# Optimization experiments

Measured on AMD Instinct MI355X. Metric: run time of the kernel, lower is better.

The kernel has to match this reference:

```python
import jax, jax.numpy as jnp
import numpy as np
from jax import lax

E = 4      # n_experts
K = 2      # top_k
D = 1024   # d_model
B, S = 4, 4096


def setup_inputs() -> dict:
    key = jax.random.key(0)
    ks = jax.random.split(key, 9)
    sc = 1.0 / np.sqrt(D)
    x = jax.random.normal(ks[0], (B, S, D), dtype=jnp.float32)
    Wg = jax.random.normal(ks[1], (E, D, D), dtype=jnp.float32) * sc
    bg = jax.random.normal(ks[2], (E, D), dtype=jnp.float32) * sc
    Wv = jax.random.normal(ks[3], (E, D, D), dtype=jnp.float32) * sc
    bv = jax.random.normal(ks[4], (E, D), dtype=jnp.float32) * sc
    Wd = jax.random.normal(ks[5], (E, D, D), dtype=jnp.float32) * sc
    # decay_bias_init = 1.0 (torch init.constant_)
    bd = jnp.ones((E, D), dtype=jnp.float32)
    Wgate = jax.random.normal(ks[7], (E, D), dtype=jnp.float32) * sc
    return {"x": x, "Wg": Wg, "bg": bg, "Wv": Wv, "bv": bv,
            "Wd": Wd, "bd": bd, "Wgate": Wgate}


def reference(x, Wg, bg, Wv, bv, Wd, bd, Wgate):
    # Per-expert projections (torch Linear: y = x @ W.T + b; W is (out,in))
    g = jnp.einsum('bsd,eod->ebso', x, Wg) + bg[:, None, None, :]  # (E,B,S,D)
    v = jnp.einsum('bsd,eod->ebso', x, Wv) + bv[:, None, None, :]
    d = jnp.einsum('bsd,eod->ebso', x, Wd) + bd[:, None, None, :]
    x_scan = jax.nn.sigmoid(g) * jnp.tanh(v)
    a = 0.001 + 0.998 * jax.nn.sigmoid(d)

    # Causal linear RNN: h_t = a_t * h_{t-1} + x_t, vectorized over (E,B,D)
    xs = jnp.moveaxis(x_scan, 2, 0)  # (S,E,B,D)
    as_ = jnp.moveaxis(a, 2, 0)      # (S,E,B,D)

    def step(h, inp):
        a_t, x_t = inp
        h = a_t * h + x_t
        return h, h

    h0 = jnp.zeros((E, B, x.shape[-1]), dtype=x.dtype)
    _, outs = lax.scan(step, h0, (as_, xs))        # (S,E,B,D)
    expert_outs = jnp.transpose(outs, (2, 0, 3, 1))  # (B,S,D,E)

    # Router: top-k experts per token, softmax over selected logits
    gate_logits = jnp.einsum('bsd,ed->bse', x, Wgate)  # (B,S,E)
    top_vals, top_idx = lax.top_k(gate_logits, K)      # (B,S,K)
    weights = jax.nn.softmax(top_vals, axis=-1)        # (B,S,K)

    idx = jnp.broadcast_to(top_idx[:, :, None, :],
                           (x.shape[0], x.shape[1], x.shape[2], K))
    selected = jnp.take_along_axis(expert_outs, idx, axis=-1)  # (B,S,D,K)
    return (selected * weights[:, :, None, :]).sum(axis=-1)
```

## Files before the change

### kernel.cpp

```cpp
#include <hip/hip_runtime.h>

#define E_EXP 4
#define D_MODEL 1024
#define B_BATCH 4
#define S_SEQ 4096
#define NTOK (B_BATCH*S_SEQ)
#define CHUNK 32
#define NCHUNK (S_SEQ/CHUNK)

typedef float f4 __attribute__((ext_vector_type(4)));
typedef float f32x4 __attribute__((ext_vector_type(4)));
typedef short bf16x8 __attribute__((ext_vector_type(8)));

__device__ __forceinline__ unsigned short f2b(float f){
  union{float f;unsigned u;}v; v.f=f;
  unsigned r = v.u + 0x7fffu + ((v.u>>16)&1u);
  return (unsigned short)(r>>16);
}
__device__ __forceinline__ float b2f_us(unsigned short v){ union{unsigned u;float f;}x; x.u=((unsigned)v)<<16; return x.f; }
__device__ __forceinline__ float b2f_lo(unsigned v){ union{unsigned u;float f;}x; x.u=v<<16; return x.f; }
__device__ __forceinline__ float b2f_hi(unsigned v){ union{unsigned u;float f;}x; x.u=v&0xffff0000u; return x.f; }

__device__ __forceinline__ void gload_lds16(const void* g, void* l){
  __builtin_amdgcn_global_load_lds(
      (const __attribute__((address_space(1))) void*)g,
      (__attribute__((address_space(3))) void*)l, 16, 0, 0);
}

__global__ __launch_bounds__(256) void cvt_bf16(const float* __restrict__ src,
                                                unsigned short* __restrict__ dst)
{
  size_t i = ((size_t)blockIdx.x*256 + threadIdx.x)*4;
  f4 v = *(const f4*)(src + i);
  ushort4 o; o.x=f2b(v[0]); o.y=f2b(v[1]); o.z=f2b(v[2]); o.w=f2b(v[3]);
  *(ushort4*)(dst + i) = o;
}

__global__ __launch_bounds__(256) void router_kernel(
    const float* __restrict__ x, const float* __restrict__ Wgate,
    float* __restrict__ wtok)
{
  int gtid = blockIdx.x*256 + threadIdx.x;
  int tok  = gtid >> 6;
  int lane = threadIdx.x & 63;
  const float* xr = x + (size_t)tok * D_MODEL;
  float acc0=0.f,acc1=0.f,acc2=0.f,acc3=0.f;
  for (int k=lane;k<D_MODEL;k+=64){
    float xv = xr[k];
    acc0 += xv*Wgate[0*D_MODEL+k];
    acc1 += xv*Wgate[1*D_MODEL+k];
    acc2 += xv*Wgate[2*D_MODEL+k];
    acc3 += xv*Wgate[3*D_MODEL+k];
  }
  #pragma unroll
  for (int off=32;off>0;off>>=1){
    acc0 += __shfl_down(acc0,off);
    acc1 += __shfl_down(acc1,off);
    acc2 += __shfl_down(acc2,off);
    acc3 += __shfl_down(acc3,off);
  }
  if (lane==0){
    float l[4]={acc0,acc1,acc2,acc3};
    int i1=0;
    #pragma unroll
    for(int e=1;e<4;e++) if (l[e]>l[i1]) i1=e;
    int i2=-1;
    #pragma unroll
    for(int e=0;e<4;e++){ if(e==i1) continue; if(i2<0||l[e]>l[i2]) i2=e; }
    float ex = __expf(l[i2]-l[i1]);
    float w1 = 1.f/(1.f+ex);
    float w2 = ex/(1.f+ex);
    float w[4]={0.f,0.f,0.f,0.f};
    w[i1]=w1; w[i2]=w2;
    float* wp = wtok + (size_t)tok*E_EXP;
    wp[0]=w[0]; wp[1]=w[1]; wp[2]=w[2]; wp[3]=w[3];
  }
}

#define BM 128
#define BN 128
#define BK 32

template<int EPI>
__global__ __launch_bounds__(256) void gemm_bf16(
    const unsigned short* __restrict__ A,
    const unsigned short* __restrict__ W,
    const float* __restrict__ bias,
    const unsigned short* __restrict__ gsrc,
    unsigned short* __restrict__ dst,
    int e0)
{
  __shared__ unsigned short sA[BM*BK];
  __shared__ unsigned short sB[BN*BK];
  int le = blockIdx.z;
  int mbase = blockIdx.x*BM, nbase = blockIdx.y*BN;
  int tid  = threadIdx.x;
  int wave = tid>>6, lane = tid&63;
  int wm = wave>>1, wn = wave&1;

  const unsigned short* We = W + (size_t)le*D_MODEL*D_MODEL;

  int srow = wave*32 + (lane>>2);
  int scol = (lane&3)*8;
  const unsigned short* gA0 = A  + (size_t)(mbase+srow)*D_MODEL + scol;
  const unsigned short* gA1 = gA0 + (size_t)16*D_MODEL;
  const unsigned short* gB0 = We + (size_t)(nbase+srow)*D_MODEL + scol;
  const unsigned short* gB1 = gB0 + (size_t)16*D_MODEL;
  unsigned short* lA0 = &sA[(wave*32)*BK];
  unsigned short* lA1 = &sA[(wave*32+16)*BK];
  unsigned short* lB0 = &sB[(wave*32)*BK];
  unsigned short* lB1 = &sB[(wave*32+16)*BK];

  f32x4 acc[4][4];
  #pragma unroll
  for (int i=0;i<4;i++)
    #pragma unroll
    for (int j=0;j<4;j++) acc[i][j] = 0;

  int arow = wm*64 + (lane&15);
  int brow = wn*64 + (lane&15);
  int kfr  = (lane>>4)*8;

  for (int k0=0; k0<D_MODEL; k0+=BK){
    gload_lds16(gA0 + k0, lA0);
    gload_lds16(gA1 + k0, lA1);
    gload_lds16(gB0 + k0, lB0);
    gload_lds16(gB1 + k0, lB1);
    __syncthreads();
    bf16x8 af[4], bfv[4];
    #pragma unroll
    for (int mi=0;mi<4;mi++) af[mi]  = *(const bf16x8*)&sA[(arow + mi*16)*BK + kfr];
    #pragma unroll
    for (int ni=0;ni<4;ni++) bfv[ni] = *(const bf16x8*)&sB[(brow + ni*16)*BK + kfr];
    #pragma unroll
    for (int mi=0;mi<4;mi++)
      #pragma unroll
      for (int ni=0;ni<4;ni++)
        acc[mi][ni] = __builtin_amdgcn_mfma_f32_16x16x32_bf16(af[mi], bfv[ni], acc[mi][ni], 0, 0, 0);
    __syncthreads();
  }

  const float* be = bias + (size_t)(e0+le)*D_MODEL;
  int me = mbase + wm*64;
  int ne = nbase + wn*64;
  #pragma unroll
  for (int mi=0;mi<4;mi++){
    #pragma unroll
    for (int r=0;r<4;r++){
      int m = me + mi*16 + (lane>>4)*4 + r;
      size_t rowoff = ((size_t)le*NTOK + m)*D_MODEL;
      #pragma unroll
      for (int ni=0;ni<4;ni++){
        int n = ne + ni*16 + (lane&15);
        float val = acc[mi][ni][r] + be[n];
        float res;
        if (EPI==0){
          res = val;
        } else if (EPI==1){
          float g  = b2f_us(gsrc[rowoff+n]);
          float sg = 1.f/(1.f+__expf(-g));
          float th = 1.f - 2.f/(__expf(2.f*val)+1.f);
          res = sg*th;
        } else {
          res = 0.001f + 0.998f/(1.f+__expf(-val));
        }
        dst[rowoff+n] = f2b(res);
      }
    }
  }
}

__global__ __launch_bounds__(512) void scan_pass1(
    const unsigned short* __restrict__ xs, const unsigned short* __restrict__ aa,
    float* __restrict__ P, float* __restrict__ U)
{
  int blk = blockIdx.x;
  int c  = blk % NCHUNK;
  int b  = (blk / NCHUNK) % B_BATCH;
  int le = blk / (NCHUNK*B_BATCH);
  int d0 = threadIdx.x*2;
  size_t base = (((size_t)(le*B_BATCH + b))*S_SEQ + (size_t)c*CHUNK)*D_MODEL + d0;
  float h0=0.f,h1=0.f,p0=1.f,p1=1.f;
  #pragma unroll 4
  for (int t=0;t<CHUNK;t++){
    unsigned av = *(const unsigned*)(aa + base);
    unsigned xv = *(const unsigned*)(xs + base);
    float a0=b2f_lo(av), a1=b2f_hi(av);
    float x0=b2f_lo(xv), x1=b2f_hi(xv);
    h0 = a0*h0 + x0; h1 = a1*h1 + x1;
    p0 *= a0; p1 *= a1;
    base += D_MODEL;
  }
  size_t sidx = (((size_t)(le*B_BATCH + b))*NCHUNK + c)*D_MODEL + d0;
  P[sidx]=p0; P[sidx+1]=p1;
  U[sidx]=h0; U[sidx+1]=h1;
}

__global__ __launch_bounds__(256) void scan_pass2(
    const float* __restrict__ P, const float* __restrict__ U, float* __restrict__ Hinit)
{
  int ch = blockIdx.x*256 + threadIdx.x;
  int d  = ch & (D_MODEL-1);
  int eb = ch >> 10;
  size_t base = (size_t)eb*NCHUNK*D_MODEL + d;
  float H=0.f;
  for (int c=0;c<NCHUNK;c++){
    size_t idx = base + (size_t)c*D_MODEL;
    Hinit[idx] = H;
    H = P[idx]*H + U[idx];
  }
}

template<int G>
__global__ __launch_bounds__(512) void scan_pass3(
    const unsigned short* __restrict__ xs, const unsigned short* __restrict__ aa,
    const float* __restrict__ Hinit, const float* __restrict__ wtok,
    float* __restrict__ out, int e0)
{
  int blk = blockIdx.x;
  int c = blk % NCHUNK;
  int b = blk / NCHUNK;
  int d0 = threadIdx.x*2;
  float h[G][2];
  #pragma unroll
  for (int le=0; le<G; le++){
    size_t hi = (((size_t)(le*B_BATCH+b))*NCHUNK + c)*D_MODEL + d0;
    h[le][0]=Hinit[hi]; h[le][1]=Hinit[hi+1];
  }
  int s0 = c*CHUNK;
  for (int t=0;t<CHUNK;t++){
    size_t n = (size_t)b*S_SEQ + s0 + t;
    float o0=0.f, o1=0.f;
    #pragma unroll
    for (int le=0;le<G;le++){
      float w = wtok[n*E_EXP + e0 + le];
      size_t idx = (((size_t)(le*B_BATCH+b))*S_SEQ + (size_t)(s0 + t))*D_MODEL + d0;
      unsigned av = *(const unsigned*)(aa+idx);
      unsigned xv = *(const unsigned*)(xs+idx);
      h[le][0] = b2f_lo(av)*h[le][0] + b2f_lo(xv);
      h[le][1] = b2f_hi(av)*h[le][1] + b2f_hi(xv);
      o0 += w*h[le][0];
      o1 += w*h[le][1];
    }
    float* op = out + n*D_MODEL + d0;
    if (G == E_EXP){ op[0]=o0; op[1]=o1; }
    else           { op[0]+=o0; op[1]+=o1; }
  }
}

extern "C" void kernel_launch(void* const* d_in, const int* in_sizes, int n_in,
                              void* d_out, int out_size, void* d_ws, size_t ws_size,
                              hipStream_t stream)
{
  const float* x     = (const float*)d_in[0];
  const float* Wg    = (const float*)d_in[1];
  const float* bg    = (const float*)d_in[2];
  const float* Wv    = (const float*)d_in[3];
  const float* bv    = (const float*)d_in[4];
  const float* Wd    = (const float*)d_in[5];
  const float* bd    = (const float*)d_in[6];
  const float* Wgate = (const float*)d_in[7];
  float* out = (float*)d_out;

  const size_t DD       = (size_t)D_MODEL*D_MODEL;
  const size_t wtok_b   = (size_t)NTOK*E_EXP*4;
  const size_t xbf_b    = (size_t)NTOK*D_MODEL*2;
  const size_t w_per_e  = DD*2;
  const size_t xs_per_e = (size_t)NTOK*D_MODEL*2;
  const size_t st_per_e = (size_t)B_BATCH*NCHUNK*D_MODEL*4;

  int G = 1;
  for (int g = 4; g >= 1; g >>= 1){
    size_t need = wtok_b + xbf_b + (size_t)g*(3*w_per_e + 2*xs_per_e + 3*st_per_e);
    if (need <= ws_size){ G = g; break; }
  }

  char* wsb = (char*)d_ws;
  size_t off = 0;
  float*          wtok = (float*)(wsb+off);          off += wtok_b;
  unsigned short* xbf  = (unsigned short*)(wsb+off); off += xbf_b;
  unsigned short* Wgbf = (unsigned short*)(wsb+off); off += (size_t)G*w_per_e;
  unsigned short* Wvbf = (unsigned short*)(wsb+off); off += (size_t)G*w_per_e;
  unsigned short* Wdbf = (unsigned short*)(wsb+off); off += (size_t)G*w_per_e;
  unsigned short* xs   = (unsigned short*)(wsb+off); off += (size_t)G*xs_per_e;
  unsigned short* aa   = (unsigned short*)(wsb+off); off += (size_t)G*xs_per_e;
  float*          P    = (float*)(wsb+off);          off += (size_t)G*st_per_e;
  float*          U    = (float*)(wsb+off);          off += (size_t)G*st_per_e;
  float*          Hi   = (float*)(wsb+off);

  hipMemsetAsync(d_out, 0, (size_t)out_size*sizeof(float), stream);

  cvt_bf16<<<(unsigned)((size_t)NTOK*D_MODEL/1024), 256, 0, stream>>>(x, xbf);
  router_kernel<<<NTOK/4, 256, 0, stream>>>(x, Wgate, wtok);

  for (int e0=0; e0<E_EXP; e0+=G){
    cvt_bf16<<<(unsigned)((size_t)G*DD/1024), 256, 0, stream>>>(Wg + (size_t)e0*DD, Wgbf);
    cvt_bf16<<<(unsigned)((size_t)G*DD/1024), 256, 0, stream>>>(Wv + (size_t)e0*DD, Wvbf);
    cvt_bf16<<<(unsigned)((size_t)G*DD/1024), 256, 0, stream>>>(Wd + (size_t)e0*DD, Wdbf);

    dim3 gg(NTOK/BM, D_MODEL/BN, G);
    gemm_bf16<0><<<gg, 256, 0, stream>>>(xbf, Wgbf, bg, nullptr, aa, e0);
    gemm_bf16<1><<<gg, 256, 0, stream>>>(xbf, Wvbf, bv, aa, xs, e0);
    gemm_bf16<2><<<gg, 256, 0, stream>>>(xbf, Wdbf, bd, nullptr, aa, e0);

    scan_pass1<<<G*B_BATCH*NCHUNK, 512, 0, stream>>>(xs, aa, P, U);
    scan_pass2<<<G*B_BATCH*D_MODEL/256, 256, 0, stream>>>(P, U, Hi);
    if (G==4)      scan_pass3<4><<<B_BATCH*NCHUNK, 512, 0, stream>>>(xs, aa, Hi, wtok, out, e0);
    else if (G==2) scan_pass3<2><<<B_BATCH*NCHUNK, 512, 0, stream>>>(xs, aa, Hi, wtok, out, e0);
    else           scan_pass3<1><<<B_BATCH*NCHUNK, 512, 0, stream>>>(xs, aa, Hi, wtok, out, e0);
  }
}
```

Baseline: 956.3 us.

## Fuse gate/value/decay GEMMs into one kernel sharing A tiles

Replaces three separate per-projection GEMMs with a single kernel that loads each x tile once and computes the g, v and d accumulators together, with BN halved to 64 to hold register pressure. The epilogue computes both the scan input and the decay directly, so the g intermediate is no longer written and re-read, and aa is not written twice. The weights are converted into an interleaved per-expert concatenated buffer. It also drops the output memset by making the first expert group overwrite rather than accumulate. The cost is three accumulator sets per thread and more LDS per block, which may lower occupancy.

```diff
diff --git a/kernel.cpp b/kernel.cpp
--- a/kernel.cpp
+++ b/kernel.cpp
@@ -17,7 +17,6 @@
   unsigned r = v.u + 0x7fffu + ((v.u>>16)&1u);
   return (unsigned short)(r>>16);
 }
-__device__ __forceinline__ float b2f_us(unsigned short v){ union{unsigned u;float f;}x; x.u=((unsigned)v)<<16; return x.f; }
 __device__ __forceinline__ float b2f_lo(unsigned v){ union{unsigned u;float f;}x; x.u=v<<16; return x.f; }
 __device__ __forceinline__ float b2f_hi(unsigned v){ union{unsigned u;float f;}x; x.u=v&0xffff0000u; return x.f; }
 
@@ -34,6 +33,18 @@
   f4 v = *(const f4*)(src + i);
   ushort4 o; o.x=f2b(v[0]); o.y=f2b(v[1]); o.z=f2b(v[2]); o.w=f2b(v[3]);
   *(ushort4*)(dst + i) = o;
+}
+
+__global__ __launch_bounds__(256) void cvt_w(const float* __restrict__ W,
+                                             unsigned short* __restrict__ Wcat,
+                                             int e0, int mat)
+{
+  size_t i4 = ((size_t)blockIdx.x*256 + threadIdx.x)*4;
+  size_t le  = i4 >> 20;
+  size_t rem = i4 & ((1u<<20)-1);
+  f4 v = *(const f4*)(W + (size_t)(e0+le)*D_MODEL*D_MODEL + rem);
+  ushort4 o; o.x=f2b(v[0]); o.y=f2b(v[1]); o.z=f2b(v[2]); o.w=f2b(v[3]);
+  *(ushort4*)(Wcat + (le*3 + mat)*((size_t)D_MODEL*D_MODEL) + rem) = o;
 }
 
 __global__ __launch_bounds__(256) void router_kernel(
@@ -78,47 +89,49 @@
 }
 
 #define BM 128
-#define BN 128
+#define BN 64
 #define BK 32
 
-template<int EPI>
-__global__ __launch_bounds__(256) void gemm_bf16(
+__global__ __launch_bounds__(256) void gemm_fused(
     const unsigned short* __restrict__ A,
-    const unsigned short* __restrict__ W,
-    const float* __restrict__ bias,
-    const unsigned short* __restrict__ gsrc,
-    unsigned short* __restrict__ dst,
+    const unsigned short* __restrict__ Wcat,
+    const float* __restrict__ bg, const float* __restrict__ bv,
+    const float* __restrict__ bd,
+    unsigned short* __restrict__ xs, unsigned short* __restrict__ aa,
     int e0)
 {
   __shared__ unsigned short sA[BM*BK];
-  __shared__ unsigned short sB[BN*BK];
+  __shared__ unsigned short sB[3*BN*BK];
   int le = blockIdx.z;
   int mbase = blockIdx.x*BM, nbase = blockIdx.y*BN;
   int tid  = threadIdx.x;
   int wave = tid>>6, lane = tid&63;
   int wm = wave>>1, wn = wave&1;
 
-  const unsigned short* We = W + (size_t)le*D_MODEL*D_MODEL;
-
-  int srow = wave*32 + (lane>>2);
+  const size_t DD = (size_t)D_MODEL*D_MODEL;
+  const unsigned short* We = Wcat + (size_t)le*3*DD;
+
+  int srow = lane>>2;
   int scol = (lane&3)*8;
-  const unsigned short* gA0 = A  + (size_t)(mbase+srow)*D_MODEL + scol;
-  const unsigned short* gA1 = gA0 + (size_t)16*D_MODEL;
-  const unsigned short* gB0 = We + (size_t)(nbase+srow)*D_MODEL + scol;
-  const unsigned short* gB1 = gB0 + (size_t)16*D_MODEL;
-  unsigned short* lA0 = &sA[(wave*32)*BK];
-  unsigned short* lA1 = &sA[(wave*32+16)*BK];
-  unsigned short* lB0 = &sB[(wave*32)*BK];
-  unsigned short* lB1 = &sB[(wave*32+16)*BK];
-
-  f32x4 acc[4][4];
+  const unsigned short* gA0 = A + (size_t)(mbase + wave*16 + srow)*D_MODEL + scol;
+  const unsigned short* gA1 = gA0 + (size_t)64*D_MODEL;
+  const unsigned short* gB0 = We + 0*DD + (size_t)(nbase + wave*16 + srow)*D_MODEL + scol;
+  const unsigned short* gB1 = We + 1*DD + (size_t)(nbase + wave*16 + srow)*D_MODEL + scol;
+  const unsigned short* gB2 = We + 2*DD + (size_t)(nbase + wave*16 + srow)*D_MODEL + scol;
+  unsigned short* lA0 = &sA[(wave*16)*BK];
+  unsigned short* lA1 = &sA[(wave*16+64)*BK];
+  unsigned short* lB0 = &sB[0*BN*BK + (wave*16)*BK];
+  unsigned short* lB1 = &sB[1*BN*BK + (wave*16)*BK];
+  unsigned short* lB2 = &sB[2*BN*BK + (wave*16)*BK];
+
+  f32x4 accG[4][2], accV[4][2], accD[4][2];
   #pragma unroll
   for (int i=0;i<4;i++)
     #pragma unroll
-    for (int j=0;j<4;j++) acc[i][j] = 0;
+    for (int j=0;j<2;j++){ accG[i][j]=0; accV[i][j]=0; accD[i][j]=0; }
 
   int arow = wm*64 + (lane&15);
-  int brow = wn*64 + (lane&15);
+  int brow = wn*32 + (lane&15);
   int kfr  = (lane>>4)*8;
 
   for (int k0=0; k0<D_MODEL; k0+=BK){
@@ -126,23 +139,32 @@
     gload_lds16(gA1 + k0, lA1);
     gload_lds16(gB0 + k0, lB0);
     gload_lds16(gB1 + k0, lB1);
+    gload_lds16(gB2 + k0, lB2);
     __syncthreads();
-    bf16x8 af[4], bfv[4];
-    #pragma unroll
-    for (int mi=0;mi<4;mi++) af[mi]  = *(const bf16x8*)&sA[(arow + mi*16)*BK + kfr];
-    #pragma unroll
-    for (int ni=0;ni<4;ni++) bfv[ni] = *(const bf16x8*)&sB[(brow + ni*16)*BK + kfr];
-    #pragma unroll
-    for (int mi=0;mi<4;mi++)
+    bf16x8 af[4];
+    #pragma unroll
+    for (int mi=0;mi<4;mi++) af[mi] = *(const bf16x8*)&sA[(arow + mi*16)*BK + kfr];
+    #pragma unroll
+    for (int ni=0;ni<2;ni++){
+      bf16x8 b0 = *(const bf16x8*)&sB[0*BN*BK + (brow + ni*16)*BK + kfr];
+      bf16x8 b1 = *(const bf16x8*)&sB[1*BN*BK + (brow + ni*16)*BK + kfr];
+      bf16x8 b2 = *(const bf16x8*)&sB[2*BN*BK + (brow + ni*16)*BK + kfr];
       #pragma unroll
-      for (int ni=0;ni<4;ni++)
-        acc[mi][ni] = __builtin_amdgcn_mfma_f32_16x16x32_bf16(af[mi], bfv[ni], acc[mi][ni], 0, 0, 0);
+      for (int mi=0;mi<4;mi++){
+        accG[mi][ni] = __builtin_amdgcn_mfma_f32_16x16x32_bf16(af[mi], b0, accG[mi][ni], 0, 0, 0);
+        accV[mi][ni] = __builtin_amdgcn_mfma_f32_16x16x32_bf16(af[mi], b1, accV[mi][ni], 0, 0, 0);
+        accD[mi][ni] = __builtin_amdgcn_mfma_f32_16x16x32_bf16(af[mi], b2, accD[mi][ni], 0, 0, 0);
+      }
+    }
     __syncthreads();
   }
 
-  const float* be = bias + (size_t)(e0+le)*D_MODEL;
+  int e = e0 + le;
+  const float* bge = bg + (size_t)e*D_MODEL;
+  const float* bve = bv + (size_t)e*D_MODEL;
+  const float* bde = bd + (size_t)e*D_MODEL;
   int me = mbase + wm*64;
-  int ne = nbase + wn*64;
+  int ne = nbase + wn*32;
   #pragma unroll
   for (int mi=0;mi<4;mi++){
     #pragma unroll
@@ -150,21 +172,16 @@
       int m = me + mi*16 + (lane>>4)*4 + r;
       size_t rowoff = ((size_t)le*NTOK + m)*D_MODEL;
       #pragma unroll
-      for (int ni=0;ni<4;ni++){
+      for (int ni=0;ni<2;ni++){
         int n = ne + ni*16 + (lane&15);
-        float val = acc[mi][ni][r] + be[n];
-        float res;
-        if (EPI==0){
-          res = val;
-        } else if (EPI==1){
-          float g  = b2f_us(gsrc[rowoff+n]);
-          float sg = 1.f/(1.f+__expf(-g));
-          float th = 1.f - 2.f/(__expf(2.f*val)+1.f);
-          res = sg*th;
-        } else {
-          res = 0.001f + 0.998f/(1.f+__expf(-val));
-        }
-        dst[rowoff+n] = f2b(res);
+        float g = accG[mi][ni][r] + bge[n];
+        float v = accV[mi][ni][r] + bve[n];
+        float d = accD[mi][ni][r] + bde[n];
+        float sg = 1.f/(1.f+__expf(-g));
+        float th = 1.f - 2.f/(__expf(2.f*v)+1.f);
+        float av = 0.001f + 0.998f/(1.f+__expf(-d));
+        xs[rowoff+n] = f2b(sg*th);
+        aa[rowoff+n] = f2b(av);
       }
     }
   }
@@ -211,7 +228,7 @@
   }
 }
 
-template<int G>
+template<int G, int FIRST>
 __global__ __launch_bounds__(512) void scan_pass3(
     const unsigned short* __restrict__ xs, const unsigned short* __restrict__ aa,
     const float* __restrict__ Hinit, const float* __restrict__ wtok,
@@ -243,8 +260,8 @@
       o1 += w*h[le][1];
     }
     float* op = out + n*D_MODEL + d0;
-    if (G == E_EXP){ op[0]=o0; op[1]=o1; }
-    else           { op[0]+=o0; op[1]+=o1; }
+    if (FIRST){ op[0]=o0;  op[1]=o1;  }
+    else      { op[0]+=o0; op[1]+=o1; }
   }
 }
 
@@ -265,13 +282,13 @@
   const size_t DD       = (size_t)D_MODEL*D_MODEL;
   const size_t wtok_b   = (size_t)NTOK*E_EXP*4;
   const size_t xbf_b    = (size_t)NTOK*D_MODEL*2;
-  const size_t w_per_e  = DD*2;
+  const size_t w_per_e  = 3*DD*2;
   const size_t xs_per_e = (size_t)NTOK*D_MODEL*2;
   const size_t st_per_e = (size_t)B_BATCH*NCHUNK*D_MODEL*4;
 
   int G = 1;
   for (int g = 4; g >= 1; g >>= 1){
-    size_t need = wtok_b + xbf_b + (size_t)g*(3*w_per_e + 2*xs_per_e + 3*st_per_e);
+    size_t need = wtok_b + xbf_b + (size_t)g*(w_per_e + 2*xs_per_e + 3*st_per_e);
     if (need <= ws_size){ G = g; break; }
   }
 
@@ -279,34 +296,35 @@
   size_t off = 0;
   float*          wtok = (float*)(wsb+off);          off += wtok_b;
   unsigned short* xbf  = (unsigned short*)(wsb+off); off += xbf_b;
-  unsigned short* Wgbf = (unsigned short*)(wsb+off); off += (size_t)G*w_per_e;
-  unsigned short* Wvbf = (unsigned short*)(wsb+off); off += (size_t)G*w_per_e;
-  unsigned short* Wdbf = (unsigned short*)(wsb+off); off += (size_t)G*w_per_e;
+  unsigned short* Wcat = (unsigned short*)(wsb+off); off += (size_t)G*w_per_e;
   unsigned short* xs   = (unsigned short*)(wsb+off); off += (size_t)G*xs_per_e;
   unsigned short* aa   = (unsigned short*)(wsb+off); off += (size_t)G*xs_per_e;
   float*          P    = (float*)(wsb+off);          off += (size_t)G*st_per_e;
   float*          U    = (float*)(wsb+off);          off += (size_t)G*st_per_e;
   float*          Hi   = (float*)(wsb+off);
 
-  hipMemsetAsync(d_out, 0, (size_t)out_size*sizeof(float), stream);
-
   cvt_bf16<<<(unsigned)((size_t)NTOK*D_MODEL/1024), 256, 0, stream>>>(x, xbf);
   router_kernel<<<NTOK/4, 256, 0, stream>>>(x, Wgate, wtok);
 
   for (int e0=0; e0<E_EXP; e0+=G){
-    cvt_bf16<<<(unsigned)((size_t)G*DD/1024), 256, 0, stream>>>(Wg + (size_t)e0*DD, Wgbf);
-    cvt_bf16<<<(unsigned)((size_t)G*DD/1024), 256, 0, stream>>>(Wv + (size_t)e0*DD, Wvbf);
-    cvt_bf16<<<(unsigned)((size_t)G*DD/1024), 256, 0, stream>>>(Wd + (size_t)e0*DD, Wdbf);
+    unsigned cvg = (unsigned)((size_t)G*DD/1024);
+    cvt_w<<<cvg, 256, 0, stream>>>(Wg, Wcat, e0, 0);
+    cvt_w<<<cvg, 256, 0, stream>>>(Wv, Wcat, e0, 1);
+    cvt_w<<<cvg, 256, 0, stream>>>(Wd, Wcat, e0, 2);
 
     dim3 gg(NTOK/BM, D_MODEL/BN, G);
-    gemm_bf16<0><<<gg, 256, 0, stream>>>(xbf, Wgbf, bg, nullptr, aa, e0);
-    gemm_bf16<1><<<gg, 256, 0, stream>>>(xbf, Wvbf, bv, aa, xs, e0);
-    gemm_bf16<2><<<gg, 256, 0, stream>>>(xbf, Wdbf, bd, nullptr, aa, e0);
+    gemm_fused<<<gg, 256, 0, stream>>>(xbf, Wcat, bg, bv, bd, xs, aa, e0);
 
     scan_pass1<<<G*B_BATCH*NCHUNK, 512, 0, stream>>>(xs, aa, P, U);
     scan_pass2<<<G*B_BATCH*D_MODEL/256, 256, 0, stream>>>(P, U, Hi);
-    if (G==4)      scan_pass3<4><<<B_BATCH*NCHUNK, 512, 0, stream>>>(xs, aa, Hi, wtok, out, e0);
-    else if (G==2) scan_pass3<2><<<B_BATCH*NCHUNK, 512, 0, stream>>>(xs, aa, Hi, wtok, out, e0);
-    else           scan_pass3<1><<<B_BATCH*NCHUNK, 512, 0, stream>>>(xs, aa, Hi, wtok, out, e0);
-  }
-}
+    bool first = (e0 == 0);
+    if (G==4)      scan_pass3<4,1><<<B_BATCH*NCHUNK, 512, 0, stream>>>(xs, aa, Hi, wtok, out, e0);
+    else if (G==2){
+      if (first) scan_pass3<2,1><<<B_BATCH*NCHUNK, 512, 0, stream>>>(xs, aa, Hi, wtok, out, e0);
+      else       scan_pass3<2,0><<<B_BATCH*NCHUNK, 512, 0, stream>>>(xs, aa, Hi, wtok, out, e0);
+    } else {
+      if (first) scan_pass3<1,1><<<B_BATCH*NCHUNK, 512, 0, stream>>>(xs, aa, Hi, wtok, out, e0);
+      else       scan_pass3<1,0><<<B_BATCH*NCHUNK, 512, 0, stream>>>(xs, aa, Hi, wtok, out, e0);
+    }
+  }
+}
```

New measurement: 1.359 ms. 42.1% more time.

## Fuse three projection GEMMs into one, move activations into scan pass

Applied to the files above, without the earlier changes.

Concatenates the Wg/Wv/Wd bf16 weights and runs a single GEMM over 3×D output columns that writes raw bf16 pre-activations. Bias, sigmoid/tanh gating and the decay activation now run inside scan_pass1, which writes xs and a back in place. The GEMM also gains an XOR-swizzled LDS layout to avoid bank conflicts. The output memset is dropped by having the first expert group store instead of accumulate. The aim is fewer launches, no gsrc re-read in the epilogue and a simpler GEMM epilogue. The cost is an extra bf16 tensor (g, v, d stored separately) and more transcendental work in the scan pass.

```diff
diff --git a/kernel.cpp b/kernel.cpp
--- a/kernel.cpp
+++ b/kernel.cpp
@@ -17,7 +17,6 @@
   unsigned r = v.u + 0x7fffu + ((v.u>>16)&1u);
   return (unsigned short)(r>>16);
 }
-__device__ __forceinline__ float b2f_us(unsigned short v){ union{unsigned u;float f;}x; x.u=((unsigned)v)<<16; return x.f; }
 __device__ __forceinline__ float b2f_lo(unsigned v){ union{unsigned u;float f;}x; x.u=v<<16; return x.f; }
 __device__ __forceinline__ float b2f_hi(unsigned v){ union{unsigned u;float f;}x; x.u=v&0xffff0000u; return x.f; }
 
@@ -34,6 +33,24 @@
   f4 v = *(const f4*)(src + i);
   ushort4 o; o.x=f2b(v[0]); o.y=f2b(v[1]); o.z=f2b(v[2]); o.w=f2b(v[3]);
   *(ushort4*)(dst + i) = o;
+}
+
+__global__ __launch_bounds__(256) void cvt_w3(const float* __restrict__ Wg,
+                                              const float* __restrict__ Wv,
+                                              const float* __restrict__ Wd,
+                                              unsigned short* __restrict__ Wcat,
+                                              int e0)
+{
+  const size_t DD = (size_t)D_MODEL*D_MODEL;
+  size_t i4 = ((size_t)blockIdx.x*256 + threadIdx.x)*4;
+  size_t le3m = i4 >> 20;
+  size_t rem  = i4 & (DD-1);
+  int mat = (int)(le3m % 3);
+  int le  = (int)(le3m / 3);
+  const float* src = (mat==0 ? Wg : (mat==1 ? Wv : Wd)) + (size_t)(e0+le)*DD + rem;
+  f4 v = *(const f4*)src;
+  ushort4 o; o.x=f2b(v[0]); o.y=f2b(v[1]); o.z=f2b(v[2]); o.w=f2b(v[3]);
+  *(ushort4*)(Wcat + le3m*DD + rem) = o;
 }
 
 __global__ __launch_bounds__(256) void router_kernel(
@@ -81,31 +98,33 @@
 #define BN 128
 #define BK 32
 
-template<int EPI>
-__global__ __launch_bounds__(256) void gemm_bf16(
+__global__ __launch_bounds__(256) void gemm_3n(
     const unsigned short* __restrict__ A,
-    const unsigned short* __restrict__ W,
-    const float* __restrict__ bias,
-    const unsigned short* __restrict__ gsrc,
-    unsigned short* __restrict__ dst,
-    int e0)
+    const unsigned short* __restrict__ Wcat,
+    unsigned short* __restrict__ gvd)
 {
   __shared__ unsigned short sA[BM*BK];
   __shared__ unsigned short sB[BN*BK];
-  int le = blockIdx.z;
-  int mbase = blockIdx.x*BM, nbase = blockIdx.y*BN;
+  const size_t DD = (size_t)D_MODEL*D_MODEL;
+  const size_t ND = (size_t)NTOK*D_MODEL;
+
+  int le    = blockIdx.z;
+  int mbase = blockIdx.x*BM;
+  int ntile = blockIdx.y;
+  int mat   = ntile>>3;
+  int nbase = (ntile&7)*BN;
   int tid  = threadIdx.x;
   int wave = tid>>6, lane = tid&63;
   int wm = wave>>1, wn = wave&1;
 
-  const unsigned short* We = W + (size_t)le*D_MODEL*D_MODEL;
-
-  int srow = wave*32 + (lane>>2);
-  int scol = (lane&3)*8;
-  const unsigned short* gA0 = A  + (size_t)(mbase+srow)*D_MODEL + scol;
-  const unsigned short* gA1 = gA0 + (size_t)16*D_MODEL;
-  const unsigned short* gB0 = We + (size_t)(nbase+srow)*D_MODEL + scol;
-  const unsigned short* gB1 = gB0 + (size_t)16*D_MODEL;
+  const unsigned short* Wmat = Wcat + ((size_t)le*3 + mat)*DD;
+
+  int src_chunk = (lane&3) ^ ((lane>>3)&3);
+  int srow = lane>>2;
+  const unsigned short* gA0 = A    + (size_t)(mbase + wave*32 + srow)*D_MODEL + src_chunk*8;
+  const unsigned short* gA1 = gA0  + (size_t)16*D_MODEL;
+  const unsigned short* gB0 = Wmat + (size_t)(nbase + wave*32 + srow)*D_MODEL + src_chunk*8;
+  const unsigned short* gB1 = gB0  + (size_t)16*D_MODEL;
   unsigned short* lA0 = &sA[(wave*32)*BK];
   unsigned short* lA1 = &sA[(wave*32+16)*BK];
   unsigned short* lB0 = &sB[(wave*32)*BK];
@@ -117,9 +136,10 @@
     #pragma unroll
     for (int j=0;j<4;j++) acc[i][j] = 0;
 
-  int arow = wm*64 + (lane&15);
-  int brow = wn*64 + (lane&15);
-  int kfr  = (lane>>4)*8;
+  int swiz   = (lane>>1)&3;
+  int rd_chk = ((lane>>4) ^ swiz)*8;
+  int a_base = (wm*64 + (lane&15))*BK + rd_chk;
+  int b_base = (wn*64 + (lane&15))*BK + rd_chk;
 
   for (int k0=0; k0<D_MODEL; k0+=BK){
     gload_lds16(gA0 + k0, lA0);
@@ -129,9 +149,9 @@
     __syncthreads();
     bf16x8 af[4], bfv[4];
     #pragma unroll
-    for (int mi=0;mi<4;mi++) af[mi]  = *(const bf16x8*)&sA[(arow + mi*16)*BK + kfr];
-    #pragma unroll
-    for (int ni=0;ni<4;ni++) bfv[ni] = *(const bf16x8*)&sB[(brow + ni*16)*BK + kfr];
+    for (int mi=0;mi<4;mi++) af[mi]  = *(const bf16x8*)&sA[a_base + mi*16*BK];
+    #pragma unroll
+    for (int ni=0;ni<4;ni++) bfv[ni] = *(const bf16x8*)&sB[b_base + ni*16*BK];
     #pragma unroll
     for (int mi=0;mi<4;mi++)
       #pragma unroll
@@ -140,7 +160,7 @@
     __syncthreads();
   }
 
-  const float* be = bias + (size_t)(e0+le)*D_MODEL;
+  unsigned short* outp = gvd + ((size_t)le*3 + mat)*ND;
   int me = mbase + wm*64;
   int ne = nbase + wn*64;
   #pragma unroll
@@ -148,47 +168,53 @@
     #pragma unroll
     for (int r=0;r<4;r++){
       int m = me + mi*16 + (lane>>4)*4 + r;
-      size_t rowoff = ((size_t)le*NTOK + m)*D_MODEL;
+      size_t rowoff = (size_t)m*D_MODEL;
       #pragma unroll
       for (int ni=0;ni<4;ni++){
         int n = ne + ni*16 + (lane&15);
-        float val = acc[mi][ni][r] + be[n];
-        float res;
-        if (EPI==0){
-          res = val;
-        } else if (EPI==1){
-          float g  = b2f_us(gsrc[rowoff+n]);
-          float sg = 1.f/(1.f+__expf(-g));
-          float th = 1.f - 2.f/(__expf(2.f*val)+1.f);
-          res = sg*th;
-        } else {
-          res = 0.001f + 0.998f/(1.f+__expf(-val));
-        }
-        dst[rowoff+n] = f2b(res);
+        outp[rowoff+n] = f2b(acc[mi][ni][r]);
       }
     }
   }
 }
 
 __global__ __launch_bounds__(512) void scan_pass1(
-    const unsigned short* __restrict__ xs, const unsigned short* __restrict__ aa,
-    float* __restrict__ P, float* __restrict__ U)
-{
+    unsigned short* __restrict__ gvd,
+    const float* __restrict__ bg, const float* __restrict__ bv, const float* __restrict__ bd,
+    float* __restrict__ P, float* __restrict__ U, int e0)
+{
+  const size_t ND = (size_t)NTOK*D_MODEL;
   int blk = blockIdx.x;
   int c  = blk % NCHUNK;
   int b  = (blk / NCHUNK) % B_BATCH;
   int le = blk / (NCHUNK*B_BATCH);
   int d0 = threadIdx.x*2;
-  size_t base = (((size_t)(le*B_BATCH + b))*S_SEQ + (size_t)c*CHUNK)*D_MODEL + d0;
+  int e  = e0 + le;
+
+  float bg0 = bg[(size_t)e*D_MODEL+d0], bg1 = bg[(size_t)e*D_MODEL+d0+1];
+  float bv0 = bv[(size_t)e*D_MODEL+d0], bv1 = bv[(size_t)e*D_MODEL+d0+1];
+  float bd0 = bd[(size_t)e*D_MODEL+d0], bd1 = bd[(size_t)e*D_MODEL+d0+1];
+
+  unsigned short* gp = gvd + (size_t)le*3*ND;
+  size_t base = (((size_t)b)*S_SEQ + (size_t)c*CHUNK)*D_MODEL + d0;
   float h0=0.f,h1=0.f,p0=1.f,p1=1.f;
-  #pragma unroll 4
   for (int t=0;t<CHUNK;t++){
-    unsigned av = *(const unsigned*)(aa + base);
-    unsigned xv = *(const unsigned*)(xs + base);
-    float a0=b2f_lo(av), a1=b2f_hi(av);
-    float x0=b2f_lo(xv), x1=b2f_hi(xv);
+    unsigned gw = *(const unsigned*)(gp + base);
+    unsigned vw = *(const unsigned*)(gp + ND + base);
+    unsigned dw = *(const unsigned*)(gp + 2*ND + base);
+    float g0 = b2f_lo(gw)+bg0, g1 = b2f_hi(gw)+bg1;
+    float v0 = b2f_lo(vw)+bv0, v1 = b2f_hi(vw)+bv1;
+    float dd0 = b2f_lo(dw)+bd0, dd1 = b2f_hi(dw)+bd1;
+    float x0 = (1.f/(1.f+__expf(-g0))) * (1.f - 2.f/(__expf(2.f*v0)+1.f));
+    float x1 = (1.f/(1.f+__expf(-g1))) * (1.f - 2.f/(__expf(2.f*v1)+1.f));
+    float a0 = 0.001f + 0.998f/(1.f+__expf(-dd0));
+    float a1 = 0.001f + 0.998f/(1.f+__expf(-dd1));
     h0 = a0*h0 + x0; h1 = a1*h1 + x1;
     p0 *= a0; p1 *= a1;
+    unsigned xsw = (unsigned)f2b(x0) | ((unsigned)f2b(x1)<<16);
+    unsigned aaw = (unsigned)f2b(a0) | ((unsigned)f2b(a1)<<16);
+    *(unsigned*)(gp + base)        = xsw;
+    *(unsigned*)(gp + 2*ND + base) = aaw;
     base += D_MODEL;
   }
   size_t sidx = (((size_t)(le*B_BATCH + b))*NCHUNK + c)*D_MODEL + d0;
@@ -211,12 +237,13 @@
   }
 }
 
-template<int G>
+template<int G, int FIRST>
 __global__ __launch_bounds__(512) void scan_pass3(
-    const unsigned short* __restrict__ xs, const unsigned short* __restrict__ aa,
+    const unsigned short* __restrict__ gvd,
     const float* __restrict__ Hinit, const float* __restrict__ wtok,
     float* __restrict__ out, int e0)
 {
+  const size_t ND = (size_t)NTOK*D_MODEL;
   int blk = blockIdx.x;
   int c = blk % NCHUNK;
   int b = blk / NCHUNK;
@@ -234,17 +261,17 @@
     #pragma unroll
     for (int le=0;le<G;le++){
       float w = wtok[n*E_EXP + e0 + le];
-      size_t idx = (((size_t)(le*B_BATCH+b))*S_SEQ + (size_t)(s0 + t))*D_MODEL + d0;
-      unsigned av = *(const unsigned*)(aa+idx);
-      unsigned xv = *(const unsigned*)(xs+idx);
+      size_t idx = (size_t)le*3*ND + n*D_MODEL + d0;
+      unsigned xv = *(const unsigned*)(gvd + idx);
+      unsigned av = *(const unsigned*)(gvd + 2*ND + idx);
       h[le][0] = b2f_lo(av)*h[le][0] + b2f_lo(xv);
       h[le][1] = b2f_hi(av)*h[le][1] + b2f_hi(xv);
       o0 += w*h[le][0];
       o1 += w*h[le][1];
     }
     float* op = out + n*D_MODEL + d0;
-    if (G == E_EXP){ op[0]=o0; op[1]=o1; }
-    else           { op[0]+=o0; op[1]+=o1; }
+    if (FIRST){ op[0]=o0;  op[1]=o1;  }
+    else      { op[0]+=o0; op[1]+=o1; }
   }
 }
 
@@ -262,16 +289,17 @@
   const float* Wgate = (const float*)d_in[7];
   float* out = (float*)d_out;
 
-  const size_t DD       = (size_t)D_MODEL*D_MODEL;
-  const size_t wtok_b   = (size_t)NTOK*E_EXP*4;
-  const size_t xbf_b    = (size_t)NTOK*D_MODEL*2;
-  const size_t w_per_e  = DD*2;
-  const size_t xs_per_e = (size_t)NTOK*D_MODEL*2;
-  const size_t st_per_e = (size_t)B_BATCH*NCHUNK*D_MODEL*4;
+  const size_t DD        = (size_t)D_MODEL*D_MODEL;
+  const size_t ND        = (size_t)NTOK*D_MODEL;
+  const size_t wtok_b    = (size_t)NTOK*E_EXP*4;
+  const size_t xbf_b     = ND*2;
+  const size_t w_per_e   = 3*DD*2;
+  const size_t gvd_per_e = 3*ND*2;
+  const size_t st_per_e  = (size_t)B_BATCH*NCHUNK*D_MODEL*4;
 
   int G = 1;
   for (int g = 4; g >= 1; g >>= 1){
-    size_t need = wtok_b + xbf_b + (size_t)g*(3*w_per_e + 2*xs_per_e + 3*st_per_e);
+    size_t need = wtok_b + xbf_b + (size_t)g*(w_per_e + gvd_per_e + 3*st_per_e);
     if (need <= ws_size){ G = g; break; }
   }
 
@@ -279,34 +307,31 @@
   size_t off = 0;
   float*          wtok = (float*)(wsb+off);          off += wtok_b;
   unsigned short* xbf  = (unsigned short*)(wsb+off); off += xbf_b;
-  unsigned short* Wgbf = (unsigned short*)(wsb+off); off += (size_t)G*w_per_e;
-  unsigned short* Wvbf = (unsigned short*)(wsb+off); off += (size_t)G*w_per_e;
-  unsigned short* Wdbf = (unsigned short*)(wsb+off); off += (size_t)G*w_per_e;
-  unsigned short* xs   = (unsigned short*)(wsb+off); off += (size_t)G*xs_per_e;
-  unsigned short* aa   = (unsigned short*)(wsb+off); off += (size_t)G*xs_per_e;
+  unsigned short* Wcat = (unsigned short*)(wsb+off); off += (size_t)G*w_per_e;
+  unsigned short* gvd  = (unsigned short*)(wsb+off); off += (size_t)G*gvd_per_e;
   float*          P    = (float*)(wsb+off);          off += (size_t)G*st_per_e;
   float*          U    = (float*)(wsb+off);          off += (size_t)G*st_per_e;
   float*          Hi   = (float*)(wsb+off);
 
-  hipMemsetAsync(d_out, 0, (size_t)out_size*sizeof(float), stream);
-
-  cvt_bf16<<<(unsigned)((size_t)NTOK*D_MODEL/1024), 256, 0, stream>>>(x, xbf);
+  cvt_bf16<<<(unsigned)(ND/1024), 256, 0, stream>>>(x, xbf);
   router_kernel<<<NTOK/4, 256, 0, stream>>>(x, Wgate, wtok);
 
   for (int e0=0; e0<E_EXP; e0+=G){
-    cvt_bf16<<<(unsigned)((size_t)G*DD/1024), 256, 0, stream>>>(Wg + (size_t)e0*DD, Wgbf);
-    cvt_bf16<<<(unsigned)((size_t)G*DD/1024), 256, 0, stream>>>(Wv + (size_t)e0*DD, Wvbf);
-    cvt_bf16<<<(unsigned)((size_t)G*DD/1024), 256, 0, stream>>>(Wd + (size_t)e0*DD, Wdbf);
-
-    dim3 gg(NTOK/BM, D_MODEL/BN, G);
-    gemm_bf16<0><<<gg, 256, 0, stream>>>(xbf, Wgbf, bg, nullptr, aa, e0);
-    gemm_bf16<1><<<gg, 256, 0, stream>>>(xbf, Wvbf, bv, aa, xs, e0);
-    gemm_bf16<2><<<gg, 256, 0, stream>>>(xbf, Wdbf, bd, nullptr, aa, e0);
-
-    scan_pass1<<<G*B_BATCH*NCHUNK, 512, 0, stream>>>(xs, aa, P, U);
+    cvt_w3<<<(unsigned)((size_t)G*3*DD/1024), 256, 0, stream>>>(Wg, Wv, Wd, Wcat, e0);
+
+    dim3 gg(NTOK/BM, 3*D_MODEL/BN, G);
+    gemm_3n<<<gg, 256, 0, stream>>>(xbf, Wcat, gvd);
+
+    scan_pass1<<<G*B_BATCH*NCHUNK, 512, 0, stream>>>(gvd, bg, bv, bd, P, U, e0);
     scan_pass2<<<G*B_BATCH*D_MODEL/256, 256, 0, stream>>>(P, U, Hi);
-    if (G==4)      scan_pass3<4><<<B_BATCH*NCHUNK, 512, 0, stream>>>(xs, aa, Hi, wtok, out, e0);
-    else if (G==2) scan_pass3<2><<<B_BATCH*NCHUNK, 512, 0, stream>>>(xs, aa, Hi, wtok, out, e0);
-    else           scan_pass3<1><<<B_BATCH*NCHUNK, 512, 0, stream>>>(xs, aa, Hi, wtok, out, e0);
-  }
-}
+    bool first = (e0 == 0);
+    if (G==4)      scan_pass3<4,1><<<B_BATCH*NCHUNK, 512, 0, stream>>>(gvd, Hi, wtok, out, e0);
+    else if (G==2){
+      if (first) scan_pass3<2,1><<<B_BATCH*NCHUNK, 512, 0, stream>>>(gvd, Hi, wtok, out, e0);
+      else       scan_pass3<2,0><<<B_BATCH*NCHUNK, 512, 0, stream>>>(gvd, Hi, wtok, out, e0);
+    } else {
+      if (first) scan_pass3<1,1><<<B_BATCH*NCHUNK, 512, 0, stream>>>(gvd, Hi, wtok, out, e0);
+      else       scan_pass3<1,0><<<B_BATCH*NCHUNK, 512, 0, stream>>>(gvd, Hi, wtok, out, e0);
+    }
+  }
+}
```

Result: faster. 905.2 us (-5.3%).
